# Kernel optimization log

Measured on AMD Instinct MI355X. Metric: run time of the kernel, lower is better.

The kernel has to match this reference:

```python
import jax, jax.numpy as jnp
import numpy as np

N_NODES = 100000
N_EDGES = 1600000
D = 128
NUM_GRAPHS = 256


def setup_inputs() -> dict:
    key = jax.random.key(0)
    ks = jax.random.split(key, 8)
    x = jax.random.normal(ks[0], (N_NODES, D), dtype=jnp.float32)
    edge_index = jax.random.randint(ks[1], (2, N_EDGES), 0, N_NODES, dtype=jnp.int32)
    edge_attr = jax.random.normal(ks[2], (N_EDGES, D), dtype=jnp.float32) * 0.1
    batch = jnp.sort(jax.random.randint(ks[3], (N_NODES,), 0, NUM_GRAPHS, dtype=jnp.int32))
    primary = jax.random.randint(ks[4], (N_NODES,), 0, 2, dtype=jnp.int32)  # 1=primary, 0=condition
    scale = 1.0 / np.sqrt(D)
    W1 = jax.random.normal(ks[5], (D, D), dtype=jnp.float32) * scale
    b1 = jnp.zeros((D,), dtype=jnp.float32)
    W2 = jax.random.normal(ks[6], (D, D), dtype=jnp.float32) * scale
    b2 = jnp.zeros((D,), dtype=jnp.float32)
    return {"x": x, "edge_index": edge_index, "edge_attr": edge_attr,
            "batch": batch, "primary": primary,
            "W1": W1, "b1": b1, "W2": W2, "b2": b2}


def reference(x, edge_index, edge_attr, batch, primary, W1, b1, W2, b2):
    n = x.shape[0]
    # --- GIN-style GNN layer: node_rep = MLP(x + sum_{e:(s->d)} (x[s] + e_attr)) ---
    src, dst = edge_index[0], edge_index[1]
    msg = x[src] + edge_attr                                  # [E, D] gather (memory-bound)
    agg = jax.ops.segment_sum(msg, dst, num_segments=n)       # [N, D] scatter-add
    h = jax.nn.relu((x + agg) @ W1 + b1) @ W2 + b2            # [N, D]

    # --- per-graph mean pool over condition nodes (primary == 0) ---
    cond = (primary == 0)
    condf = cond.astype(h.dtype)[:, None]
    csum = jax.ops.segment_sum(h * condf, batch, num_segments=NUM_GRAPHS)   # [G, D]
    ccnt = jax.ops.segment_sum(condf, batch, num_segments=NUM_GRAPHS)       # [G, 1]
    # graphs with no condition nodes get a zero pool (matches torch branch)
    pool = jnp.where(ccnt > 0, csum / jnp.maximum(ccnt, 1.0), 0.0)          # [G, D]

    # --- assemble rows: per graph, primary rows [h | cond_pool] first, then zero rows
    # for condition nodes (matches the torch concat order) ---
    key = batch * 2 + cond.astype(batch.dtype)      # primary nodes sort before condition nodes
    order = jnp.argsort(key, stable=True)
    h_o = h[order]                                   # [N, D]
    pool_o = pool[batch[order]]                      # [N, D]
    prim_o = (primary[order] == 1)[:, None]
    out = jnp.where(prim_o, jnp.concatenate([h_o, pool_o], axis=1), 0.0)    # [N, 2D]
    return out
```

## Files before the change

### kernel.cpp

```cpp
#include <hip/hip_runtime.h>

#define D 128
#define NG 256

typedef __attribute__((ext_vector_type(8))) short bf16x8;
typedef __attribute__((ext_vector_type(4))) float f32x4;

__device__ inline ushort f2bf(float f) {
  uint b = __float_as_uint(f);
  return (ushort)((b + 0x7fffu + ((b >> 16) & 1u)) >> 16);
}

__global__ __launch_bounds__(256) void deg_kernel(const int* __restrict__ ei,
                                                  int* __restrict__ deg, int E) {
  int e = blockIdx.x * blockDim.x + threadIdx.x;
  if (e < E) atomicAdd(&deg[ei[E + e]], 1);
}

__global__ __launch_bounds__(256) void scan_block_sums(const int* __restrict__ deg,
                                                       int* __restrict__ bsum, int N) {
  __shared__ int red[256];
  int t = threadIdx.x;
  int base = blockIdx.x * 1024;
  int s = 0;
#pragma unroll
  for (int j = 0; j < 4; ++j) {
    int i = base + t * 4 + j;
    if (i < N) s += deg[i];
  }
  red[t] = s;
  __syncthreads();
  for (int o = 128; o > 0; o >>= 1) {
    if (t < o) red[t] += red[t + o];
    __syncthreads();
  }
  if (t == 0) bsum[blockIdx.x] = red[0];
}

__global__ void scan_bsum(int* __restrict__ bsum, int nb) {
  if (threadIdx.x == 0) {
    int run = 0;
    for (int i = 0; i < nb; ++i) {
      int v = bsum[i];
      bsum[i] = run;
      run += v;
    }
  }
}

__global__ __launch_bounds__(256) void scan_final(const int* __restrict__ deg,
                                                  const int* __restrict__ bsum,
                                                  int* __restrict__ off, int N) {
  __shared__ int ts[256];
  int t = threadIdx.x;
  int base = blockIdx.x * 1024;
  int v[4];
  int s = 0;
#pragma unroll
  for (int j = 0; j < 4; ++j) {
    int i = base + t * 4 + j;
    v[j] = (i < N) ? deg[i] : 0;
    s += v[j];
  }
  ts[t] = s;
  __syncthreads();
  for (int o = 1; o < 256; o <<= 1) {
    int u = (t >= o) ? ts[t - o] : 0;
    __syncthreads();
    ts[t] += u;
    __syncthreads();
  }
  int excl = ts[t] - s + bsum[blockIdx.x];
#pragma unroll
  for (int j = 0; j < 4; ++j) {
    int i = base + t * 4 + j;
    if (i < N) off[i] = excl;
    excl += v[j];
    if (i == N - 1) off[N] = excl;
  }
}

__global__ __launch_bounds__(256) void fill_kernel(const int* __restrict__ ei,
                                                   const int* __restrict__ off,
                                                   int* __restrict__ cursor,
                                                   int2* __restrict__ csr, int E) {
  int e = blockIdx.x * blockDim.x + threadIdx.x;
  if (e >= E) return;
  int d = ei[E + e];
  int slot = atomicAdd(&cursor[d], 1);
  csr[off[d] + slot] = make_int2(ei[e], e);
}

__global__ __launch_bounds__(256) void cvt_kernel(const float* __restrict__ x,
                                                  ushort* __restrict__ xb, int total4) {
  int i = blockIdx.x * blockDim.x + threadIdx.x;
  if (i >= total4) return;
  float4 v = ((const float4*)x)[i];
  ushort4 o;
  o.x = f2bf(v.x); o.y = f2bf(v.y); o.z = f2bf(v.z); o.w = f2bf(v.w);
  ((ushort4*)xb)[i] = o;
}

__global__ __launch_bounds__(256) void cvtW_kernel(const float* __restrict__ W1,
                                                   const float* __restrict__ W2,
                                                   ushort* __restrict__ W1T,
                                                   ushort* __restrict__ W2T) {
  int idx = blockIdx.x * blockDim.x + threadIdx.x;
  int w = idx >> 14;
  int k = (idx >> 7) & 127;
  int n = idx & 127;
  const float* src = w ? W2 : W1;
  ushort* dst = w ? W2T : W1T;
  dst[n * 128 + k] = f2bf(src[k * 128 + n]);
}

__global__ __launch_bounds__(256) void gather_kernel(const ushort* __restrict__ xb,
                                                     const float* __restrict__ ea,
                                                     const int2* __restrict__ csr,
                                                     const int* __restrict__ off,
                                                     ushort* __restrict__ yb, int N) {
  long long tid = (long long)blockIdx.x * blockDim.x + threadIdx.x;
  int n = (int)(tid >> 5);
  int c = (int)(tid & 31);
  if (n >= N) return;
  const float4* ea4 = (const float4*)ea;
  const ushort4* xb4 = (const ushort4*)xb;
  ushort4 self = xb4[(size_t)n * 32 + c];
  float4 acc = make_float4(__uint_as_float((uint)self.x << 16),
                           __uint_as_float((uint)self.y << 16),
                           __uint_as_float((uint)self.z << 16),
                           __uint_as_float((uint)self.w << 16));
  int s = off[n], e = off[n + 1];
  int k = s;
  for (; k + 2 <= e; k += 2) {
    int2 p0 = csr[k];
    int2 p1 = csr[k + 1];
    float4 a0 = ea4[(size_t)p0.y * 32 + c];
    float4 a1 = ea4[(size_t)p1.y * 32 + c];
    ushort4 u0 = xb4[(size_t)p0.x * 32 + c];
    ushort4 u1 = xb4[(size_t)p1.x * 32 + c];
    acc.x += a0.x + __uint_as_float((uint)u0.x << 16);
    acc.y += a0.y + __uint_as_float((uint)u0.y << 16);
    acc.z += a0.z + __uint_as_float((uint)u0.z << 16);
    acc.w += a0.w + __uint_as_float((uint)u0.w << 16);
    acc.x += a1.x + __uint_as_float((uint)u1.x << 16);
    acc.y += a1.y + __uint_as_float((uint)u1.y << 16);
    acc.z += a1.z + __uint_as_float((uint)u1.z << 16);
    acc.w += a1.w + __uint_as_float((uint)u1.w << 16);
  }
  if (k < e) {
    int2 p0 = csr[k];
    float4 a0 = ea4[(size_t)p0.y * 32 + c];
    ushort4 u0 = xb4[(size_t)p0.x * 32 + c];
    acc.x += a0.x + __uint_as_float((uint)u0.x << 16);
    acc.y += a0.y + __uint_as_float((uint)u0.y << 16);
    acc.z += a0.z + __uint_as_float((uint)u0.z << 16);
    acc.w += a0.w + __uint_as_float((uint)u0.w << 16);
  }
  ushort4 o;
  o.x = f2bf(acc.x); o.y = f2bf(acc.y); o.z = f2bf(acc.z); o.w = f2bf(acc.w);
  ((ushort4*)yb)[(size_t)n * 32 + c] = o;
}

__global__ void counts_kernel(const int* __restrict__ batch, const int* __restrict__ primary,
                              int* __restrict__ ncount, int* __restrict__ ccnt, int N) {
  int n = blockIdx.x * blockDim.x + threadIdx.x;
  if (n >= N) return;
  int g = batch[n];
  atomicAdd(&ncount[g], 1);
  if (primary[n] == 0) atomicAdd(&ccnt[g], 1);
}

__global__ __launch_bounds__(256) void mlp_mfma_kernel(
    const ushort* __restrict__ yb, float* __restrict__ h,
    const ushort* __restrict__ W1T, const float* __restrict__ b1,
    const ushort* __restrict__ W2T, const float* __restrict__ b2,
    const int* __restrict__ batch, const int* __restrict__ primary,
    float* __restrict__ csum, int N) {
  __shared__ ushort tl[4][16][D];
  __shared__ float csl[4][D];
  const int tid = threadIdx.x;
  const int w = tid >> 6;
  const int l = tid & 63;
  const int lr = l & 15;
  const int lg = l >> 4;
  const int base = blockIdx.x * 64;
  const int m0 = base + w * 16;

  for (int i = tid; i < 4 * D; i += 256) ((float*)csl)[i] = 0.f;
  int gmin = batch[base < N ? base : N - 1];
  __syncthreads();

  f32x4 acc[8];
#pragma unroll
  for (int t = 0; t < 8; ++t) {
    float bv = b1[t * 16 + lr];
    acc[t][0] = bv; acc[t][1] = bv; acc[t][2] = bv; acc[t][3] = bv;
  }
  int arow = m0 + lr;
  if (arow >= N) arow = N - 1;
#pragma unroll
  for (int kk = 0; kk < 4; ++kk) {
    bf16x8 a = *(const bf16x8*)&yb[(size_t)arow * D + kk * 32 + lg * 8];
#pragma unroll
    for (int t = 0; t < 8; ++t) {
      bf16x8 b = *(const bf16x8*)&W1T[(size_t)(t * 16 + lr) * D + kk * 32 + lg * 8];
      acc[t] = __builtin_amdgcn_mfma_f32_16x16x32_bf16(a, b, acc[t], 0, 0, 0);
    }
  }
#pragma unroll
  for (int t = 0; t < 8; ++t) {
#pragma unroll
    for (int r = 0; r < 4; ++r) {
      float v = acc[t][r];
      v = v > 0.f ? v : 0.f;
      int m = lg * 4 + r;
      int col = (t * 16 + lr) ^ ((m & 7) << 3);
      tl[w][m][col] = f2bf(v);
    }
  }
  __syncthreads();

  f32x4 acc2[8];
#pragma unroll
  for (int t = 0; t < 8; ++t) {
    float bv = b2[t * 16 + lr];
    acc2[t][0] = bv; acc2[t][1] = bv; acc2[t][2] = bv; acc2[t][3] = bv;
  }
#pragma unroll
  for (int kk = 0; kk < 4; ++kk) {
    bf16x8 a = *(const bf16x8*)&tl[w][lr][(kk * 32 + lg * 8) ^ ((lr & 7) << 3)];
#pragma unroll
    for (int t = 0; t < 8; ++t) {
      bf16x8 b = *(const bf16x8*)&W2T[(size_t)(t * 16 + lr) * D + kk * 32 + lg * 8];
      acc2[t] = __builtin_amdgcn_mfma_f32_16x16x32_bf16(a, b, acc2[t], 0, 0, 0);
    }
  }

#pragma unroll
  for (int r = 0; r < 4; ++r) {
    int m = m0 + lg * 4 + r;
    if (m >= N) continue;
    bool cond = (primary[m] == 0);
    int g = batch[m];
    int gl = g - gmin;
#pragma unroll
    for (int t = 0; t < 8; ++t) {
      float v = acc2[t][r];
      h[(size_t)m * D + t * 16 + lr] = v;
      if (cond) {
        if (gl < 4) atomicAdd(&csl[gl][t * 16 + lr], v);
        else unsafeAtomicAdd(&csum[(size_t)g * D + t * 16 + lr], v);
      }
    }
  }
  __syncthreads();
  for (int i = tid; i < 4 * D; i += 256) {
    float v = ((float*)csl)[i];
    if (v != 0.f) {
      int gl = i >> 7, c = i & 127;
      unsafeAtomicAdd(&csum[(size_t)(gmin + gl) * D + c], v);
    }
  }
}

__global__ void scan_kernel(const int* __restrict__ ncount, int* __restrict__ gstart) {
  __shared__ int a[NG];
  int tx = threadIdx.x;
  int v = ncount[tx];
  a[tx] = v;
  __syncthreads();
  for (int off = 1; off < NG; off <<= 1) {
    int u = (tx >= off) ? a[tx - off] : 0;
    __syncthreads();
    a[tx] += u;
    __syncthreads();
  }
  gstart[tx] = a[tx] - v;
  if (tx == NG - 1) gstart[NG] = a[tx];
}

__global__ void pool_kernel(const float* __restrict__ csum, const int* __restrict__ ccnt,
                            float* __restrict__ pool) {
  int g = blockIdx.x, c = threadIdx.x;
  int cnt = ccnt[g];
  pool[(size_t)g * D + c] = cnt > 0 ? csum[(size_t)g * D + c] / (float)cnt : 0.0f;
}

__global__ __launch_bounds__(256) void rank_kernel(const int* __restrict__ primary,
                                                   const int* __restrict__ gstart,
                                                   const int* __restrict__ ccnt,
                                                   int* __restrict__ pos) {
  int g = blockIdx.x;
  int s = gstart[g], e = gstart[g + 1];
  int pcnt = (e - s) - ccnt[g];
  __shared__ int wcntP[4], wcntC[4];
  int prun = 0, crun = 0;
  for (int i0 = s; i0 < e; i0 += 256) {
    int n = i0 + threadIdx.x;
    bool valid = n < e;
    int isP = (valid && primary[n] == 1) ? 1 : 0;
    int isC = (valid && primary[n] != 1) ? 1 : 0;
    unsigned long long mP = __ballot(isP);
    unsigned long long mC = __ballot(isC);
    int lane = threadIdx.x & 63;
    int wid = threadIdx.x >> 6;
    if (lane == 0) { wcntP[wid] = __popcll(mP); wcntC[wid] = __popcll(mC); }
    __syncthreads();
    int preP = __popcll(mP & ((1ULL << lane) - 1ULL));
    int preC = __popcll(mC & ((1ULL << lane) - 1ULL));
    int woffP = 0, woffC = 0;
#pragma unroll
    for (int ww = 0; ww < 4; ++ww)
      if (ww < wid) { woffP += wcntP[ww]; woffC += wcntC[ww]; }
    int totP = wcntP[0] + wcntP[1] + wcntP[2] + wcntP[3];
    int totC = wcntC[0] + wcntC[1] + wcntC[2] + wcntC[3];
    if (valid) {
      if (isP)
        pos[n] = s + prun + woffP + preP;
      else
        pos[n] = ~(s + pcnt + crun + woffC + preC);
    }
    prun += totP;
    crun += totC;
    __syncthreads();
  }
}

__global__ __launch_bounds__(256) void write_kernel(
    const float* __restrict__ h, const float* __restrict__ pool,
    const int* __restrict__ batch, const int* __restrict__ pos,
    float* __restrict__ out, int N) {
  long long tid = (long long)blockIdx.x * blockDim.x + threadIdx.x;
  int n = (int)(tid >> 6);
  int c = (int)(tid & 63);
  if (n >= N) return;
  int p = pos[n];
  float4 v = make_float4(0.f, 0.f, 0.f, 0.f);
  int pp;
  if (p >= 0) {
    pp = p;
    if (c < 32)
      v = ((const float4*)h)[(size_t)n * 32 + c];
    else
      v = ((const float4*)pool)[(size_t)batch[n] * 32 + (c - 32)];
  } else {
    pp = ~p;
  }
  ((float4*)out)[(size_t)pp * 64 + c] = v;
}

extern "C" void kernel_launch(void* const* d_in, const int* in_sizes, int n_in,
                              void* d_out, int out_size, void* d_ws, size_t ws_size,
                              hipStream_t stream) {
  const float* x = (const float*)d_in[0];
  const int* ei = (const int*)d_in[1];
  const float* ea = (const float*)d_in[2];
  const int* batch = (const int*)d_in[3];
  const int* primary = (const int*)d_in[4];
  const float* W1 = (const float*)d_in[5];
  const float* b1 = (const float*)d_in[6];
  const float* W2 = (const float*)d_in[7];
  const float* b2 = (const float*)d_in[8];
  float* out = (float*)d_out;

  const int N = in_sizes[0] / D;
  const int E = in_sizes[1] / 2;
  const int nb = (N + 1023) / 1024;

  float* h = (float*)d_ws;
  float* csum = h + (size_t)N * D;
  float* pool = csum + (size_t)NG * D;
  ushort* yb = (ushort*)(pool + (size_t)NG * D);
  ushort* xb = yb + (size_t)N * D;
  ushort* W1T = xb + (size_t)N * D;
  ushort* W2T = W1T + D * D;
  int2* csr = (int2*)(W2T + D * D);
  int* ip = (int*)(csr + (size_t)E);
  int* deg = ip;
  int* off = deg + N;
  int* cursor = off + N + 4;
  int* bsum = cursor + N;
  int* ccnt = bsum + 128;
  int* ncount = ccnt + NG;
  int* gstart = ncount + NG;
  int* pos = gstart + 260;

  hipMemsetAsync(csum, 0, (size_t)NG * D * 4, stream);
  hipMemsetAsync(deg, 0, (size_t)N * 4, stream);
  hipMemsetAsync(cursor, 0, (size_t)N * 4, stream);
  hipMemsetAsync(ccnt, 0, (size_t)NG * 2 * 4, stream);

  deg_kernel<<<(E + 255) / 256, 256, 0, stream>>>(ei, deg, E);
  scan_block_sums<<<nb, 256, 0, stream>>>(deg, bsum, N);
  scan_bsum<<<1, 64, 0, stream>>>(bsum, nb);
  scan_final<<<nb, 256, 0, stream>>>(deg, bsum, off, N);
  fill_kernel<<<(E + 255) / 256, 256, 0, stream>>>(ei, off, cursor, csr, E);
  cvt_kernel<<<((N * D / 4) + 255) / 256, 256, 0, stream>>>(x, xb, N * D / 4);
  cvtW_kernel<<<(2 * D * D + 255) / 256, 256, 0, stream>>>(W1, W2, W1T, W2T);
  {
    long long threads = (long long)N * 32;
    gather_kernel<<<(int)((threads + 255) / 256), 256, 0, stream>>>(xb, ea, csr, off, yb, N);
  }
  counts_kernel<<<(N + 255) / 256, 256, 0, stream>>>(batch, primary, ncount, ccnt, N);
  mlp_mfma_kernel<<<(N + 63) / 64, 256, 0, stream>>>(yb, h, W1T, b1, W2T, b2, batch, primary,
                                                     csum, N);
  scan_kernel<<<1, NG, 0, stream>>>(ncount, gstart);
  pool_kernel<<<NG, D, 0, stream>>>(csum, ccnt, pool);
  rank_kernel<<<NG, 256, 0, stream>>>(primary, gstart, ccnt, pos);
  write_kernel<<<(int)(((long long)N * 64 + 255) / 256), 256, 0, stream>>>(h, pool, batch, pos,
                                                                           out, N);
}
```

Before: 664.2 us.

## Fuse MLP output directly into permuted rows and merge small kernels

The MLP kernel now runs after the rank computation and writes h straight into its permuted output row, zeroing condition rows. This removes the intermediate h buffer and the separate write pass. A new pool-write kernel fills only the pooled half of primary rows, and the pool normalisation is folded into it. Degree and count kernels are merged, the two conversion kernels are merged, the gather is unrolled by four, and nontemporal loads and stores are added. The MLP output stores are strided scalar writes to scattered rows, which may coalesce less well than the old float4 copy.

```diff
diff --git a/kernel.cpp b/kernel.cpp
--- a/kernel.cpp
+++ b/kernel.cpp
@@ -5,16 +5,32 @@
 
 typedef __attribute__((ext_vector_type(8))) short bf16x8;
 typedef __attribute__((ext_vector_type(4))) float f32x4;
+typedef __attribute__((ext_vector_type(4))) float f4;
+typedef __attribute__((ext_vector_type(2))) int i2;
+typedef __attribute__((ext_vector_type(4))) ushort u16x4;
 
 __device__ inline ushort f2bf(float f) {
   uint b = __float_as_uint(f);
   return (ushort)((b + 0x7fffu + ((b >> 16) & 1u)) >> 16);
 }
-
-__global__ __launch_bounds__(256) void deg_kernel(const int* __restrict__ ei,
-                                                  int* __restrict__ deg, int E) {
+__device__ inline float bf2f(ushort u) { return __uint_as_float((uint)u << 16); }
+
+__global__ __launch_bounds__(256) void deg_counts_kernel(const int* __restrict__ ei,
+                                                         int* __restrict__ deg,
+                                                         const int* __restrict__ batch,
+                                                         const int* __restrict__ primary,
+                                                         int* __restrict__ ncount,
+                                                         int* __restrict__ ccnt, int E, int N) {
   int e = blockIdx.x * blockDim.x + threadIdx.x;
-  if (e < E) atomicAdd(&deg[ei[E + e]], 1);
+  if (e < E) {
+    int d = __builtin_nontemporal_load(&ei[E + e]);
+    atomicAdd(&deg[d], 1);
+  }
+  if (e < N) {
+    int g = batch[e];
+    atomicAdd(&ncount[g], 1);
+    if (primary[e] == 0) atomicAdd(&ccnt[g], 1);
+  }
 }
 
 __global__ __launch_bounds__(256) void scan_block_sums(const int* __restrict__ deg,
@@ -83,185 +99,100 @@
 __global__ __launch_bounds__(256) void fill_kernel(const int* __restrict__ ei,
                                                    const int* __restrict__ off,
                                                    int* __restrict__ cursor,
-                                                   int2* __restrict__ csr, int E) {
+                                                   i2* __restrict__ csr, int E) {
   int e = blockIdx.x * blockDim.x + threadIdx.x;
   if (e >= E) return;
-  int d = ei[E + e];
+  int s = __builtin_nontemporal_load(&ei[e]);
+  int d = __builtin_nontemporal_load(&ei[E + e]);
   int slot = atomicAdd(&cursor[d], 1);
-  csr[off[d] + slot] = make_int2(ei[e], e);
+  i2 v;
+  v.x = s;
+  v.y = e;
+  __builtin_nontemporal_store(v, &csr[off[d] + slot]);
 }
 
 __global__ __launch_bounds__(256) void cvt_kernel(const float* __restrict__ x,
-                                                  ushort* __restrict__ xb, int total4) {
+                                                  ushort* __restrict__ xb,
+                                                  const float* __restrict__ W1,
+                                                  const float* __restrict__ W2,
+                                                  ushort* __restrict__ W1T,
+                                                  ushort* __restrict__ W2T, int total4) {
   int i = blockIdx.x * blockDim.x + threadIdx.x;
-  if (i >= total4) return;
-  float4 v = ((const float4*)x)[i];
-  ushort4 o;
-  o.x = f2bf(v.x); o.y = f2bf(v.y); o.z = f2bf(v.z); o.w = f2bf(v.w);
-  ((ushort4*)xb)[i] = o;
-}
-
-__global__ __launch_bounds__(256) void cvtW_kernel(const float* __restrict__ W1,
-                                                   const float* __restrict__ W2,
-                                                   ushort* __restrict__ W1T,
-                                                   ushort* __restrict__ W2T) {
-  int idx = blockIdx.x * blockDim.x + threadIdx.x;
-  int w = idx >> 14;
-  int k = (idx >> 7) & 127;
-  int n = idx & 127;
-  const float* src = w ? W2 : W1;
-  ushort* dst = w ? W2T : W1T;
-  dst[n * 128 + k] = f2bf(src[k * 128 + n]);
+  if (i < total4) {
+    f4 v = __builtin_nontemporal_load(&((const f4*)x)[i]);
+    u16x4 o;
+    o.x = f2bf(v.x);
+    o.y = f2bf(v.y);
+    o.z = f2bf(v.z);
+    o.w = f2bf(v.w);
+    ((u16x4*)xb)[i] = o;
+  }
+  if (i < 2 * D * D) {
+    int w = i >> 14;
+    int k = (i >> 7) & 127;
+    int n = i & 127;
+    const float* src = w ? W2 : W1;
+    ushort* dst = w ? W2T : W1T;
+    dst[n * 128 + k] = f2bf(src[k * 128 + n]);
+  }
 }
 
 __global__ __launch_bounds__(256) void gather_kernel(const ushort* __restrict__ xb,
                                                      const float* __restrict__ ea,
-                                                     const int2* __restrict__ csr,
+                                                     const i2* __restrict__ csr,
                                                      const int* __restrict__ off,
                                                      ushort* __restrict__ yb, int N) {
   long long tid = (long long)blockIdx.x * blockDim.x + threadIdx.x;
   int n = (int)(tid >> 5);
   int c = (int)(tid & 31);
   if (n >= N) return;
-  const float4* ea4 = (const float4*)ea;
-  const ushort4* xb4 = (const ushort4*)xb;
-  ushort4 self = xb4[(size_t)n * 32 + c];
-  float4 acc = make_float4(__uint_as_float((uint)self.x << 16),
-                           __uint_as_float((uint)self.y << 16),
-                           __uint_as_float((uint)self.z << 16),
-                           __uint_as_float((uint)self.w << 16));
+  const f4* ea4 = (const f4*)ea;
+  const u16x4* xb4 = (const u16x4*)xb;
+  u16x4 self = xb4[(size_t)n * 32 + c];
+  f4 acc;
+  acc.x = bf2f(self.x);
+  acc.y = bf2f(self.y);
+  acc.z = bf2f(self.z);
+  acc.w = bf2f(self.w);
   int s = off[n], e = off[n + 1];
   int k = s;
-  for (; k + 2 <= e; k += 2) {
-    int2 p0 = csr[k];
-    int2 p1 = csr[k + 1];
-    float4 a0 = ea4[(size_t)p0.y * 32 + c];
-    float4 a1 = ea4[(size_t)p1.y * 32 + c];
-    ushort4 u0 = xb4[(size_t)p0.x * 32 + c];
-    ushort4 u1 = xb4[(size_t)p1.x * 32 + c];
-    acc.x += a0.x + __uint_as_float((uint)u0.x << 16);
-    acc.y += a0.y + __uint_as_float((uint)u0.y << 16);
-    acc.z += a0.z + __uint_as_float((uint)u0.z << 16);
-    acc.w += a0.w + __uint_as_float((uint)u0.w << 16);
-    acc.x += a1.x + __uint_as_float((uint)u1.x << 16);
-    acc.y += a1.y + __uint_as_float((uint)u1.y << 16);
-    acc.z += a1.z + __uint_as_float((uint)u1.z << 16);
-    acc.w += a1.w + __uint_as_float((uint)u1.w << 16);
-  }
-  if (k < e) {
-    int2 p0 = csr[k];
-    float4 a0 = ea4[(size_t)p0.y * 32 + c];
-    ushort4 u0 = xb4[(size_t)p0.x * 32 + c];
-    acc.x += a0.x + __uint_as_float((uint)u0.x << 16);
-    acc.y += a0.y + __uint_as_float((uint)u0.y << 16);
-    acc.z += a0.z + __uint_as_float((uint)u0.z << 16);
-    acc.w += a0.w + __uint_as_float((uint)u0.w << 16);
-  }
-  ushort4 o;
-  o.x = f2bf(acc.x); o.y = f2bf(acc.y); o.z = f2bf(acc.z); o.w = f2bf(acc.w);
-  ((ushort4*)yb)[(size_t)n * 32 + c] = o;
-}
-
-__global__ void counts_kernel(const int* __restrict__ batch, const int* __restrict__ primary,
-                              int* __restrict__ ncount, int* __restrict__ ccnt, int N) {
-  int n = blockIdx.x * blockDim.x + threadIdx.x;
-  if (n >= N) return;
-  int g = batch[n];
-  atomicAdd(&ncount[g], 1);
-  if (primary[n] == 0) atomicAdd(&ccnt[g], 1);
-}
-
-__global__ __launch_bounds__(256) void mlp_mfma_kernel(
-    const ushort* __restrict__ yb, float* __restrict__ h,
-    const ushort* __restrict__ W1T, const float* __restrict__ b1,
-    const ushort* __restrict__ W2T, const float* __restrict__ b2,
-    const int* __restrict__ batch, const int* __restrict__ primary,
-    float* __restrict__ csum, int N) {
-  __shared__ ushort tl[4][16][D];
-  __shared__ float csl[4][D];
-  const int tid = threadIdx.x;
-  const int w = tid >> 6;
-  const int l = tid & 63;
-  const int lr = l & 15;
-  const int lg = l >> 4;
-  const int base = blockIdx.x * 64;
-  const int m0 = base + w * 16;
-
-  for (int i = tid; i < 4 * D; i += 256) ((float*)csl)[i] = 0.f;
-  int gmin = batch[base < N ? base : N - 1];
-  __syncthreads();
-
-  f32x4 acc[8];
-#pragma unroll
-  for (int t = 0; t < 8; ++t) {
-    float bv = b1[t * 16 + lr];
-    acc[t][0] = bv; acc[t][1] = bv; acc[t][2] = bv; acc[t][3] = bv;
-  }
-  int arow = m0 + lr;
-  if (arow >= N) arow = N - 1;
-#pragma unroll
-  for (int kk = 0; kk < 4; ++kk) {
-    bf16x8 a = *(const bf16x8*)&yb[(size_t)arow * D + kk * 32 + lg * 8];
-#pragma unroll
-    for (int t = 0; t < 8; ++t) {
-      bf16x8 b = *(const bf16x8*)&W1T[(size_t)(t * 16 + lr) * D + kk * 32 + lg * 8];
-      acc[t] = __builtin_amdgcn_mfma_f32_16x16x32_bf16(a, b, acc[t], 0, 0, 0);
-    }
-  }
-#pragma unroll
-  for (int t = 0; t < 8; ++t) {
-#pragma unroll
-    for (int r = 0; r < 4; ++r) {
-      float v = acc[t][r];
-      v = v > 0.f ? v : 0.f;
-      int m = lg * 4 + r;
-      int col = (t * 16 + lr) ^ ((m & 7) << 3);
-      tl[w][m][col] = f2bf(v);
-    }
-  }
-  __syncthreads();
-
-  f32x4 acc2[8];
-#pragma unroll
-  for (int t = 0; t < 8; ++t) {
-    float bv = b2[t * 16 + lr];
-    acc2[t][0] = bv; acc2[t][1] = bv; acc2[t][2] = bv; acc2[t][3] = bv;
-  }
-#pragma unroll
-  for (int kk = 0; kk < 4; ++kk) {
-    bf16x8 a = *(const bf16x8*)&tl[w][lr][(kk * 32 + lg * 8) ^ ((lr & 7) << 3)];
-#pragma unroll
-    for (int t = 0; t < 8; ++t) {
-      bf16x8 b = *(const bf16x8*)&W2T[(size_t)(t * 16 + lr) * D + kk * 32 + lg * 8];
-      acc2[t] = __builtin_amdgcn_mfma_f32_16x16x32_bf16(a, b, acc2[t], 0, 0, 0);
-    }
-  }
-
-#pragma unroll
-  for (int r = 0; r < 4; ++r) {
-    int m = m0 + lg * 4 + r;
-    if (m >= N) continue;
-    bool cond = (primary[m] == 0);
-    int g = batch[m];
-    int gl = g - gmin;
-#pragma unroll
-    for (int t = 0; t < 8; ++t) {
-      float v = acc2[t][r];
-      h[(size_t)m * D + t * 16 + lr] = v;
-      if (cond) {
-        if (gl < 4) atomicAdd(&csl[gl][t * 16 + lr], v);
-        else unsafeAtomicAdd(&csum[(size_t)g * D + t * 16 + lr], v);
-      }
-    }
-  }
-  __syncthreads();
-  for (int i = tid; i < 4 * D; i += 256) {
-    float v = ((float*)csl)[i];
-    if (v != 0.f) {
-      int gl = i >> 7, c = i & 127;
-      unsafeAtomicAdd(&csum[(size_t)(gmin + gl) * D + c], v);
-    }
-  }
+  for (; k + 4 <= e; k += 4) {
+    i2 p0 = __builtin_nontemporal_load(&csr[k]);
+    i2 p1 = __builtin_nontemporal_load(&csr[k + 1]);
+    i2 p2 = __builtin_nontemporal_load(&csr[k + 2]);
+    i2 p3 = __builtin_nontemporal_load(&csr[k + 3]);
+    f4 a0 = __builtin_nontemporal_load(&ea4[(size_t)p0.y * 32 + c]);
+    f4 a1 = __builtin_nontemporal_load(&ea4[(size_t)p1.y * 32 + c]);
+    f4 a2 = __builtin_nontemporal_load(&ea4[(size_t)p2.y * 32 + c]);
+    f4 a3 = __builtin_nontemporal_load(&ea4[(size_t)p3.y * 32 + c]);
+    u16x4 u0 = xb4[(size_t)p0.x * 32 + c];
+    u16x4 u1 = xb4[(size_t)p1.x * 32 + c];
+    u16x4 u2 = xb4[(size_t)p2.x * 32 + c];
+    u16x4 u3 = xb4[(size_t)p3.x * 32 + c];
+    acc.x += (a0.x + bf2f(u0.x)) + (a1.x + bf2f(u1.x));
+    acc.y += (a0.y + bf2f(u0.y)) + (a1.y + bf2f(u1.y));
+    acc.z += (a0.z + bf2f(u0.z)) + (a1.z + bf2f(u1.z));
+    acc.w += (a0.w + bf2f(u0.w)) + (a1.w + bf2f(u1.w));
+    acc.x += (a2.x + bf2f(u2.x)) + (a3.x + bf2f(u3.x));
+    acc.y += (a2.y + bf2f(u2.y)) + (a3.y + bf2f(u3.y));
+    acc.z += (a2.z + bf2f(u2.z)) + (a3.z + bf2f(u3.z));
+    acc.w += (a2.w + bf2f(u2.w)) + (a3.w + bf2f(u3.w));
+  }
+  for (; k < e; ++k) {
+    i2 p0 = __builtin_nontemporal_load(&csr[k]);
+    f4 a0 = __builtin_nontemporal_load(&ea4[(size_t)p0.y * 32 + c]);
+    u16x4 u0 = xb4[(size_t)p0.x * 32 + c];
+    acc.x += a0.x + bf2f(u0.x);
+    acc.y += a0.y + bf2f(u0.y);
+    acc.z += a0.z + bf2f(u0.z);
+    acc.w += a0.w + bf2f(u0.w);
+  }
+  u16x4 o;
+  o.x = f2bf(acc.x);
+  o.y = f2bf(acc.y);
+  o.z = f2bf(acc.z);
+  o.w = f2bf(acc.w);
+  __builtin_nontemporal_store(o, &((u16x4*)yb)[(size_t)n * 32 + c]);
 }
 
 __global__ void scan_kernel(const int* __restrict__ ncount, int* __restrict__ gstart) {
@@ -278,13 +209,6 @@
   }
   gstart[tx] = a[tx] - v;
   if (tx == NG - 1) gstart[NG] = a[tx];
-}
-
-__global__ void pool_kernel(const float* __restrict__ csum, const int* __restrict__ ccnt,
-                            float* __restrict__ pool) {
-  int g = blockIdx.x, c = threadIdx.x;
-  int cnt = ccnt[g];
-  pool[(size_t)g * D + c] = cnt > 0 ? csum[(size_t)g * D + c] / (float)cnt : 0.0f;
 }
 
 __global__ __launch_bounds__(256) void rank_kernel(const int* __restrict__ primary,
@@ -327,27 +251,131 @@
   }
 }
 
-__global__ __launch_bounds__(256) void write_kernel(
-    const float* __restrict__ h, const float* __restrict__ pool,
-    const int* __restrict__ batch, const int* __restrict__ pos,
-    float* __restrict__ out, int N) {
+__global__ __launch_bounds__(256) void mlp_mfma_kernel(
+    const ushort* __restrict__ yb, float* __restrict__ out,
+    const ushort* __restrict__ W1T, const float* __restrict__ b1,
+    const ushort* __restrict__ W2T, const float* __restrict__ b2,
+    const int* __restrict__ batch, const int* __restrict__ primary,
+    const int* __restrict__ pos, float* __restrict__ csum, int N) {
+  __shared__ ushort tl[4][16][D];
+  __shared__ float csl[4][D];
+  const int tid = threadIdx.x;
+  const int w = tid >> 6;
+  const int l = tid & 63;
+  const int lr = l & 15;
+  const int lg = l >> 4;
+  const int base = blockIdx.x * 64;
+  const int m0 = base + w * 16;
+
+  for (int i = tid; i < 4 * D; i += 256) ((float*)csl)[i] = 0.f;
+  int gmin = batch[base < N ? base : N - 1];
+  __syncthreads();
+
+  f32x4 acc[8];
+#pragma unroll
+  for (int t = 0; t < 8; ++t) {
+    float bv = b1[t * 16 + lr];
+    acc[t][0] = bv; acc[t][1] = bv; acc[t][2] = bv; acc[t][3] = bv;
+  }
+  int arow = m0 + lr;
+  if (arow >= N) arow = N - 1;
+#pragma unroll
+  for (int kk = 0; kk < 4; ++kk) {
+    bf16x8 a = *(const bf16x8*)&yb[(size_t)arow * D + kk * 32 + lg * 8];
+#pragma unroll
+    for (int t = 0; t < 8; ++t) {
+      bf16x8 b = *(const bf16x8*)&W1T[(size_t)(t * 16 + lr) * D + kk * 32 + lg * 8];
+      acc[t] = __builtin_amdgcn_mfma_f32_16x16x32_bf16(a, b, acc[t], 0, 0, 0);
+    }
+  }
+#pragma unroll
+  for (int t = 0; t < 8; ++t) {
+#pragma unroll
+    for (int r = 0; r < 4; ++r) {
+      float v = acc[t][r];
+      v = v > 0.f ? v : 0.f;
+      int m = lg * 4 + r;
+      int col = (t * 16 + lr) ^ ((m & 7) << 3);
+      tl[w][m][col] = f2bf(v);
+    }
+  }
+  __syncthreads();
+
+  f32x4 acc2[8];
+#pragma unroll
+  for (int t = 0; t < 8; ++t) {
+    float bv = b2[t * 16 + lr];
+    acc2[t][0] = bv; acc2[t][1] = bv; acc2[t][2] = bv; acc2[t][3] = bv;
+  }
+#pragma unroll
+  for (int kk = 0; kk < 4; ++kk) {
+    bf16x8 a = *(const bf16x8*)&tl[w][lr][(kk * 32 + lg * 8) ^ ((lr & 7) << 3)];
+#pragma unroll
+    for (int t = 0; t < 8; ++t) {
+      bf16x8 b = *(const bf16x8*)&W2T[(size_t)(t * 16 + lr) * D + kk * 32 + lg * 8];
+      acc2[t] = __builtin_amdgcn_mfma_f32_16x16x32_bf16(a, b, acc2[t], 0, 0, 0);
+    }
+  }
+
+#pragma unroll
+  for (int r = 0; r < 4; ++r) {
+    int m = m0 + lg * 4 + r;
+    if (m >= N) continue;
+    int p = pos[m];
+    if (p >= 0) {
+      size_t ro = (size_t)p * 256;
+#pragma unroll
+      for (int t = 0; t < 8; ++t)
+        __builtin_nontemporal_store(acc2[t][r], &out[ro + t * 16 + lr]);
+    } else {
+      size_t ro = (size_t)(~p) * 256;
+#pragma unroll
+      for (int t = 0; t < 8; ++t) {
+        __builtin_nontemporal_store(0.0f, &out[ro + t * 16 + lr]);
+        __builtin_nontemporal_store(0.0f, &out[ro + 128 + t * 16 + lr]);
+      }
+      int g = batch[m];
+      int gl = g - gmin;
+      if (gl < 4) {
+#pragma unroll
+        for (int t = 0; t < 8; ++t) atomicAdd(&csl[gl][t * 16 + lr], acc2[t][r]);
+      } else {
+#pragma unroll
+        for (int t = 0; t < 8; ++t)
+          unsafeAtomicAdd(&csum[(size_t)g * D + t * 16 + lr], acc2[t][r]);
+      }
+    }
+  }
+  __syncthreads();
+  for (int i = tid; i < 4 * D; i += 256) {
+    float v = ((float*)csl)[i];
+    if (v != 0.f) {
+      int gl = i >> 7, c = i & 127;
+      unsafeAtomicAdd(&csum[(size_t)(gmin + gl) * D + c], v);
+    }
+  }
+}
+
+__global__ __launch_bounds__(256) void poolwrite_kernel(const float* __restrict__ csum,
+                                                        const int* __restrict__ ccnt,
+                                                        const int* __restrict__ batch,
+                                                        const int* __restrict__ pos,
+                                                        float* __restrict__ out, int N) {
   long long tid = (long long)blockIdx.x * blockDim.x + threadIdx.x;
-  int n = (int)(tid >> 6);
-  int c = (int)(tid & 63);
+  int n = (int)(tid >> 5);
+  int c = (int)(tid & 31);
   if (n >= N) return;
   int p = pos[n];
-  float4 v = make_float4(0.f, 0.f, 0.f, 0.f);
-  int pp;
-  if (p >= 0) {
-    pp = p;
-    if (c < 32)
-      v = ((const float4*)h)[(size_t)n * 32 + c];
-    else
-      v = ((const float4*)pool)[(size_t)batch[n] * 32 + (c - 32)];
-  } else {
-    pp = ~p;
-  }
-  ((float4*)out)[(size_t)pp * 64 + c] = v;
+  if (p < 0) return;
+  int g = batch[n];
+  int cnt = ccnt[g];
+  f4 v = {0.f, 0.f, 0.f, 0.f};
+  if (cnt > 0) {
+    f4 s4 = ((const f4*)csum)[(size_t)g * 32 + c];
+    float inv = 1.0f / (float)cnt;
+    v = s4 * inv;
+  }
+  __builtin_nontemporal_store(v, &((f4*)out)[(size_t)p * 64 + 32 + c]);
 }
 
 extern "C" void kernel_launch(void* const* d_in, const int* in_sizes, int n_in,
@@ -368,14 +396,12 @@
   const int E = in_sizes[1] / 2;
   const int nb = (N + 1023) / 1024;
 
-  float* h = (float*)d_ws;
-  float* csum = h + (size_t)N * D;
-  float* pool = csum + (size_t)NG * D;
-  ushort* yb = (ushort*)(pool + (size_t)NG * D);
+  float* csum = (float*)d_ws;
+  ushort* yb = (ushort*)(csum + (size_t)NG * D);
   ushort* xb = yb + (size_t)N * D;
   ushort* W1T = xb + (size_t)N * D;
   ushort* W2T = W1T + D * D;
-  int2* csr = (int2*)(W2T + D * D);
+  i2* csr = (i2*)(W2T + D * D);
   int* ip = (int*)(csr + (size_t)E);
   int* deg = ip;
   int* off = deg + N;
@@ -391,23 +417,21 @@
   hipMemsetAsync(cursor, 0, (size_t)N * 4, stream);
   hipMemsetAsync(ccnt, 0, (size_t)NG * 2 * 4, stream);
 
-  deg_kernel<<<(E + 255) / 256, 256, 0, stream>>>(ei, deg, E);
+  deg_counts_kernel<<<(E + 255) / 256, 256, 0, stream>>>(ei, deg, batch, primary, ncount, ccnt,
+                                                         E, N);
   scan_block_sums<<<nb, 256, 0, stream>>>(deg, bsum, N);
   scan_bsum<<<1, 64, 0, stream>>>(bsum, nb);
   scan_final<<<nb, 256, 0, stream>>>(deg, bsum, off, N);
   fill_kernel<<<(E + 255) / 256, 256, 0, stream>>>(ei, off, cursor, csr, E);
-  cvt_kernel<<<((N * D / 4) + 255) / 256, 256, 0, stream>>>(x, xb, N * D / 4);
-  cvtW_kernel<<<(2 * D * D + 255) / 256, 256, 0, stream>>>(W1, W2, W1T, W2T);
+  cvt_kernel<<<((N * D / 4) + 255) / 256, 256, 0, stream>>>(x, xb, W1, W2, W1T, W2T, N * D / 4);
   {
     long long threads = (long long)N * 32;
     gather_kernel<<<(int)((threads + 255) / 256), 256, 0, stream>>>(xb, ea, csr, off, yb, N);
   }
-  counts_kernel<<<(N + 255) / 256, 256, 0, stream>>>(batch, primary, ncount, ccnt, N);
-  mlp_mfma_kernel<<<(N + 63) / 64, 256, 0, stream>>>(yb, h, W1T, b1, W2T, b2, batch, primary,
-                                                     csum, N);
   scan_kernel<<<1, NG, 0, stream>>>(ncount, gstart);
-  pool_kernel<<<NG, D, 0, stream>>>(csum, ccnt, pool);
   rank_kernel<<<NG, 256, 0, stream>>>(primary, gstart, ccnt, pos);
-  write_kernel<<<(int)(((long long)N * 64 + 255) / 256), 256, 0, stream>>>(h, pool, batch, pos,
-                                                                           out, N);
-}
+  mlp_mfma_kernel<<<(N + 63) / 64, 256, 0, stream>>>(yb, out, W1T, b1, W2T, b2, batch, primary,
+                                                     pos, csum, N);
+  poolwrite_kernel<<<(int)(((long long)N * 32 + 255) / 256), 256, 0, stream>>>(csum, ccnt, batch,
+                                                                               pos, out, N);
+}
```

Measured after the change: 648.2 us. 1.02x faster.
